# Kernel tuning notes

Hardware: AMD Instinct MI355X
Metric: run time of the kernel (lower is better)

Reference implementation:

```python
import jax, jax.numpy as jnp
import numpy as np

CODEBOOK_SIZE = 1024
LATENT_DIM = 256
COMMITMENT_COST = 0.25
EMA_DECAY = 0.99
EPS = 1e-05


def setup_inputs() -> dict:
    key = jax.random.key(0)
    k1, k2, k3 = jax.random.split(key, 3)
    B, D, T, K = 32, LATENT_DIM, 2048, CODEBOOK_SIZE
    z = jax.random.normal(k1, (B, D, T), dtype=jnp.float32)
    embedding = jax.random.normal(k2, (K, D), dtype=jnp.float32) * (1.0 / K)
    ema_count = jnp.ones((K,), dtype=jnp.float32)
    ema_weight = jax.random.normal(k3, (K, D), dtype=jnp.float32) * (1.0 / K)
    return {"z": z, "embedding": embedding, "ema_count": ema_count, "ema_weight": ema_weight}


def reference(z, embedding, ema_count, ema_weight):
    B, D, T = z.shape
    K = embedding.shape[0]
    # (B, D, T) -> (B*T, D)
    z_flat = jnp.transpose(z, (0, 2, 1)).reshape(-1, D)

    # Squared L2 distances: ||z||^2 + ||e||^2 - 2 z.e
    d = (jnp.sum(z_flat * z_flat, axis=1, keepdims=True)
         + jnp.sum(embedding * embedding, axis=1)[None, :]
         - 2.0 * (z_flat @ embedding.T))  # (N, K)
    token_ids_flat = jnp.argmin(d, axis=1)  # (N,)
    z_q_flat = embedding[token_ids_flat]    # (N, D)

    # Losses (stop_gradient mirrors .detach())
    commitment_loss = jnp.mean((z_flat - jax.lax.stop_gradient(z_q_flat)) ** 2)
    codebook_loss = jnp.mean((z_q_flat - jax.lax.stop_gradient(z_flat)) ** 2)
    vq_loss = codebook_loss + COMMITMENT_COST * commitment_loss

    # Straight-through estimator
    z_q_flat_ste = z_flat + jax.lax.stop_gradient(z_q_flat - z_flat)
    z_q = jnp.transpose(z_q_flat_ste.reshape(B, T, D), (0, 2, 1))
    token_ids = token_ids_flat.reshape(B, T)

    # EMA codebook update (training-mode, no-grad)
    zf = jax.lax.stop_gradient(z_flat)
    ids = jax.lax.stop_gradient(token_ids_flat)
    counts = jax.ops.segment_sum(jnp.ones_like(zf[:, 0]), ids, num_segments=K)  # (K,)
    sums = jax.ops.segment_sum(zf, ids, num_segments=K)                          # (K, D)
    new_ema_count = EMA_DECAY * ema_count + (1.0 - EMA_DECAY) * counts
    new_ema_weight = EMA_DECAY * ema_weight + (1.0 - EMA_DECAY) * sums
    n = jnp.sum(new_ema_count)
    smoothed = (new_ema_count + EPS) / (n + K * EPS) * n
    new_embedding = new_ema_weight / smoothed[:, None]

    return z_q, token_ids, vq_loss, new_embedding, new_ema_count, new_ema_weight
```

## Files before the change

kernel.cpp:

```cpp
#include <hip/hip_runtime.h>
#include <hip/hip_bf16.h>
#include <string.h>

#define D_ 256
#define K_ 1024
#define T_ 2048
#define B_ 32
#define N_ 65536

#define OFF_ZQ   0u
#define OFF_IDS  16777216u
#define OFF_LOSS 16842752u
#define OFF_EMB  16842753u
#define OFF_CNT  17104897u
#define OFF_W    17105921u

#define WS_IDS     0x000000u
#define WS_ZN      0x040000u
#define WS_ORDER   0x080000u
#define WS_SUMS    0x0C0000u
#define WS_COUNTS  0x1C0000u
#define WS_EN      0x1C1000u
#define WS_SM      0x1C2000u
#define WS_OFFS    0x1C3000u
#define WS_CURSOR  0x1C4000u
#define WS_LOSS    0x1C5000u
#define WS_END_SM  0x1C6000u
#define WS_ESPLIT  0x290000u
#define WS_TOP2    0x390000u
#define WS_ZSPLIT  0x1000000u
#define WS_END_XL  0x3000000u

#define TAU 2.0e-4f

typedef float f32x4 __attribute__((ext_vector_type(4)));
typedef _Float16 f16x8 __attribute__((ext_vector_type(8)));
typedef unsigned short ushort_t;
typedef unsigned long long u64;

static __device__ inline float fmul_rn_opaque(float a, float b) {
  float r = a * b;
  asm volatile("" : "+v"(r));
  return r;
}

static __device__ inline ushort_t f2h(float x) {
  _Float16 h = (_Float16)x;
  ushort_t u;
  __builtin_memcpy(&u, &h, 2);
  return u;
}
static __device__ inline float h2f(ushort_t u) {
  _Float16 h;
  __builtin_memcpy(&h, &u, 2);
  return (float)h;
}

static __device__ inline u64 skey(float s, int j) {
  unsigned int u = __float_as_uint(s);
  u = u ^ ((unsigned int)((int)u >> 31) | 0x80000000u);
  return ((u64)u << 32) | (unsigned int)j;
}
static __device__ inline float key_s(u64 k) {
  unsigned int u = (unsigned int)(k >> 32);
  u = (u & 0x80000000u) ? (u ^ 0x80000000u) : ~u;
  return __uint_as_float(u);
}

static __device__ __forceinline__ void gload16(const void* g, void* l) {
  __builtin_amdgcn_global_load_lds(
      (const __attribute__((address_space(1))) void*)g,
      (__attribute__((address_space(3))) void*)l, 16, 0, 0);
}

template <typename F>
static __device__ inline float np_pairwise256(F term) {
  float h0 = 0.f, h1 = 0.f;
#pragma unroll
  for (int half = 0; half < 2; ++half) {
    const int base = half * 128;
    float r[8];
#pragma unroll
    for (int k = 0; k < 8; ++k) r[k] = term(base + k);
    for (int i = 8; i < 128; i += 8) {
#pragma unroll
      for (int k = 0; k < 8; ++k) r[k] += term(base + i + k);
    }
    float v = ((r[0] + r[1]) + (r[2] + r[3])) + ((r[4] + r[5]) + (r[6] + r[7]));
    if (half == 0) h0 = v; else h1 = v;
  }
  return h0 + h1;
}

__global__ __launch_bounds__(256) void k_eprep(const float* __restrict__ emb,
                                               float* __restrict__ en,
                                               ushort_t* __restrict__ esplit) {
  const int tid = threadIdx.x;
  const int j = blockIdx.x * 32 + (tid >> 3);
  const int k = tid & 7;
  const float* e = emb + (size_t)j * D_;

  float h[2];
#pragma unroll
  for (int half = 0; half < 2; ++half) {
    float r = 0.f;
    for (int i = 0; i < 16; ++i) {
      float x = e[half * 128 + 8 * i + k];
      float t = fmul_rn_opaque(x, x);
      r = (i == 0) ? t : r + t;
    }
    float s = r + __shfl_xor(r, 1, 64);
    s = s + __shfl_xor(s, 2, 64);
    s = s + __shfl_xor(s, 4, 64);
    h[half] = s;
  }
  if (k == 0) en[j] = h[0] + h[1];

  ushort_t* er = esplit + (size_t)j * 256;
#pragma unroll
  for (int m = 0; m < 32; m += 4) {
    float4 v = *reinterpret_cast<const float4*>(e + k * 32 + m);
    *reinterpret_cast<ushort4*>(er + k * 32 + m) =
        make_ushort4(f2h(v.x * 256.f), f2h(v.y * 256.f),
                     f2h(v.z * 256.f), f2h(v.w * 256.f));
  }
}

__global__ __launch_bounds__(256) void k_zprep(const float* __restrict__ z,
                                               float* __restrict__ zn,
                                               ushort_t* __restrict__ zsplit) {
  __shared__ float tile[64][68];
  const int tid = threadIdx.x, bid = blockIdx.x;
  const int tchunk = bid & 31, b = bid >> 5;
  const int n0 = b * T_ + tchunk * 64;
  const int t4 = tid & 15, rq = tid >> 4;
  const int tok = tid >> 2, p = tid & 3;

  float r0 = 0.f, r1 = 0.f, h0 = 0.f;
  for (int c = 0; c < 4; ++c) {
    __syncthreads();
    const float* zp = z + (size_t)b * D_ * T_ + (size_t)(c * 64) * T_ + tchunk * 64;
#pragma unroll
    for (int i = 0; i < 4; ++i) {
      int dd = rq + 16 * i;
      *reinterpret_cast<float4*>(&tile[dd][t4 * 4]) =
          *reinterpret_cast<const float4*>(&zp[(size_t)dd * T_ + t4 * 4]);
    }
    __syncthreads();
    {
      ushort_t* dst = zsplit + (size_t)(n0 + tok) * 256 + c * 64 + p * 16;
      unsigned int wbuf[8];
#pragma unroll
      for (int jj = 0; jj < 16; jj += 2) {
        float x0 = tile[p * 16 + jj][tok];
        float x1 = tile[p * 16 + jj + 1][tok];
        wbuf[jj >> 1] = (unsigned int)f2h(x0) | ((unsigned int)f2h(x1) << 16);
      }
      *reinterpret_cast<uint4*>(dst) = make_uint4(wbuf[0], wbuf[1], wbuf[2], wbuf[3]);
      *reinterpret_cast<uint4*>(dst + 8) = make_uint4(wbuf[4], wbuf[5], wbuf[6], wbuf[7]);
    }
#pragma unroll
    for (int il = 0; il < 8; ++il) {
      float x0 = tile[8 * il + 2 * p][tok];
      float x1 = tile[8 * il + 2 * p + 1][tok];
      float t0 = fmul_rn_opaque(x0, x0);
      float t1 = fmul_rn_opaque(x1, x1);
      if ((c & 1) == 0 && il == 0) { r0 = t0; r1 = t1; }
      else { r0 += t0; r1 += t1; }
    }
    if (c & 1) {
      float s = r0 + r1;
      s = s + __shfl_xor(s, 1, 64);
      s = s + __shfl_xor(s, 2, 64);
      if (c == 1) h0 = s;
      else if (p == 0) zn[n0 + tok] = h0 + s;
    }
  }
}

static __device__ inline void top2merge(u64& k1, u64& k2, u64 o1, u64 o2) {
  if (o1 < k1) { u64 t = k1 < o2 ? k1 : o2; k2 = t; k1 = o1; }
  else { k2 = k2 < o1 ? k2 : o1; }
}

__global__ __launch_bounds__(512) void k_gemm(
    const ushort_t* __restrict__ zsplit, const ushort_t* __restrict__ esplit,
    const float* __restrict__ en, ulonglong2* __restrict__ top2) {
  __shared__ char ldsbuf[65536];

  const int tid = threadIdx.x;
  const int w = blockIdx.x;
  const int xcd = w & 7;
  const int local = w >> 3;
  const int tt = (xcd << 5) + (local >> 2);
  const int ct = local & 3;
  const int r0 = tt * 256, c0 = ct * 256;

  const int lane = tid & 63;
  const int wv = tid >> 6;
  const int wm = wv >> 2, wn = wv & 3;
  const int m16 = lane & 15;
  const int g = lane >> 4;
  const int gb = g << 4;

  const int rl = lane >> 3;
  const int vlane = rl * 512 + ((((lane & 7) << 4)) ^ (rl << 4));
  const char* gza = (const char*)zsplit + (size_t)(r0 + wv * 32) * 512 + vlane;
  const char* gea = (const char*)esplit + (size_t)(c0 + wv * 32) * 512 + vlane;

  f32x4 acc[8][4];
#pragma unroll
  for (int mi = 0; mi < 8; ++mi)
#pragma unroll
    for (int ni = 0; ni < 4; ++ni) acc[mi][ni] = f32x4{0.f, 0.f, 0.f, 0.f};

  auto STAGE = [&](int it_) {
    const int kb = it_ << 7;
    char* lz = ldsbuf + wv * 4096;
    char* le = ldsbuf + 32768 + wv * 4096;
    const char* ga = gza + kb;
    const char* ge = gea + kb;
#pragma unroll
    for (int i = 0; i < 4; ++i) {
      gload16(ga + i * 4096, lz + i * 1024);
      gload16(ge + i * 4096, le + i * 1024);
    }
  };

  STAGE(0);
  __builtin_amdgcn_sched_barrier(0);

  const char* Zb = ldsbuf;
  const char* Eb = ldsbuf + 32768;
  for (int it = 0; it < 4; ++it) {
    asm volatile("s_waitcnt vmcnt(0)" ::: "memory");
    __builtin_amdgcn_sched_barrier(0);
    __builtin_amdgcn_s_barrier();
    __builtin_amdgcn_sched_barrier(0);

#pragma unroll
    for (int ks = 0; ks < 2; ++ks) {
      f16x8 ef[8], zf[4];
#pragma unroll
      for (int mi = 0; mi < 8; ++mi) {
        int row = wm * 128 + mi * 16 + m16;
        ef[mi] = *reinterpret_cast<const f16x8*>(
            Eb + row * 128 + (((ks << 6) + gb) ^ ((row & 7) << 4)));
      }
#pragma unroll
      for (int ni = 0; ni < 4; ++ni) {
        int row = wn * 64 + ni * 16 + m16;
        zf[ni] = *reinterpret_cast<const f16x8*>(
            Zb + row * 128 + (((ks << 6) + gb) ^ ((row & 7) << 4)));
      }
#pragma unroll
      for (int mi = 0; mi < 8; ++mi)
#pragma unroll
        for (int ni = 0; ni < 4; ++ni)
          acc[mi][ni] = __builtin_amdgcn_mfma_f32_16x16x32_f16(
              ef[mi], zf[ni], acc[mi][ni], 0, 0, 0);
    }
    asm volatile("s_waitcnt lgkmcnt(0)" ::: "memory");
    __builtin_amdgcn_sched_barrier(0);
    __builtin_amdgcn_s_barrier();
    __builtin_amdgcn_sched_barrier(0);
    if (it < 3) STAGE(it + 1);
    __builtin_amdgcn_sched_barrier(0);
  }

  u64* pairbuf = (u64*)ldsbuf;
  float env[8][4];
#pragma unroll
  for (int mi = 0; mi < 8; ++mi)
#pragma unroll
    for (int rg = 0; rg < 4; ++rg)
      env[mi][rg] = en[c0 + wm * 128 + mi * 16 + g * 4 + rg];

#pragma unroll
  for (int ni = 0; ni < 4; ++ni) {
    const int tok = wn * 64 + ni * 16 + m16;
    u64 k1 = ~0ull, k2 = ~0ull;
#pragma unroll
    for (int mi = 0; mi < 8; ++mi) {
#pragma unroll
      for (int rg = 0; rg < 4; ++rg) {
        int j = c0 + wm * 128 + mi * 16 + g * 4 + rg;
        float s = env[mi][rg] - acc[mi][ni][rg] * 0.0078125f;
        u64 key = skey(s, j);
        if (key < k1) { k2 = k1; k1 = key; }
        else if (key < k2) { k2 = key; }
      }
    }
    u64 o1 = (u64)__shfl_xor((long long)k1, 16, 64);
    u64 o2 = (u64)__shfl_xor((long long)k2, 16, 64);
    top2merge(k1, k2, o1, o2);
    o1 = (u64)__shfl_xor((long long)k1, 32, 64);
    o2 = (u64)__shfl_xor((long long)k2, 32, 64);
    top2merge(k1, k2, o1, o2);
    if (g == 0) {
      pairbuf[(tok * 2 + wm) * 2 + 0] = k1;
      pairbuf[(tok * 2 + wm) * 2 + 1] = k2;
    }
  }
  __syncthreads();
  if (tid < 256) {
    u64 a1 = pairbuf[(tid * 2 + 0) * 2 + 0], a2 = pairbuf[(tid * 2 + 0) * 2 + 1];
    top2merge(a1, a2, pairbuf[(tid * 2 + 1) * 2 + 0], pairbuf[(tid * 2 + 1) * 2 + 1]);
    top2[(size_t)(r0 + tid) * 4 + ct] = make_ulonglong2(a1, a2);
  }
}

__global__ __launch_bounds__(256) void k_merge(
    const ulonglong2* __restrict__ top2, const float* __restrict__ z,
    const float* __restrict__ emb, const float* __restrict__ en,
    const float* __restrict__ zn, int* __restrict__ ids,
    float* __restrict__ counts, double* __restrict__ loss,
    float* __restrict__ out) {
  int n = blockIdx.x * 256 + threadIdx.x;
  const ulonglong2* tp = top2 + (size_t)n * 4;
  const float znv = zn[n];
  u64 k[8];
#pragma unroll
  for (int i = 0; i < 4; ++i) {
    ulonglong2 v = tp[i];
    k[2 * i] = v.x; k[2 * i + 1] = v.y;
  }
  u64 mn = k[0];
#pragma unroll
  for (int i = 1; i < 8; ++i) mn = k[i] < mn ? k[i] : mn;
  float lim = key_s(mn) + TAU;
  int cnt = 0;
  int cj[4] = {0, 0, 0, 0};
#pragma unroll
  for (int i = 0; i < 8; ++i) {
    if (key_s(k[i]) <= lim) {
      if (cnt < 4) cj[cnt] = (int)(k[i] & 1023u);
      cnt++;
    }
  }
  int jf;
  float loss_n;
  if (cnt == 1) {
    jf = (int)(mn & 1023u);
    loss_n = znv + key_s(mn);
  } else {
    int b = n >> 11, t = n & 2047;
    const float* zb = z + (size_t)b * (D_ * (size_t)T_) + t;
    const float* e0 = emb + (size_t)cj[0] * D_;
    const float* e1 = emb + (size_t)cj[1] * D_;
    const float* e2 = emb + (size_t)cj[2] * D_;
    const float* e3 = emb + (size_t)cj[3] * D_;
    float a0 = 0.f, a1 = 0.f, a2 = 0.f, a3 = 0.f;
    for (int d = 0; d < D_; ++d) {
      float zv = zb[(size_t)d * T_];
      a0 = fmaf(zv, e0[d], a0);
      a1 = fmaf(zv, e1[d], a1);
      a2 = fmaf(zv, e2[d], a2);
      a3 = fmaf(zv, e3[d], a3);
    }
    float av[4] = {a0, a1, a2, a3};
    u64 best = ~0ull;
#pragma unroll
    for (int c = 0; c < 4; ++c) {
      if (c < cnt) {
        float A = znv + en[cj[c]];
        float s = A - 2.0f * av[c];
        u64 key = skey(s, cj[c]);
        best = key < best ? key : best;
      }
    }
    jf = (int)(best & 1023u);
    loss_n = key_s(best);
  }
  ids[n] = jf;
  out[OFF_IDS + (unsigned)n] = (float)jf;
  unsafeAtomicAdd(&counts[jf], 1.0f);

  float acc = loss_n;
#pragma unroll
  for (int o = 32; o; o >>= 1) acc += __shfl_down(acc, o);
  __shared__ float ls[4];
  int tid = threadIdx.x;
  if ((tid & 63) == 0) ls[tid >> 6] = acc;
  __syncthreads();
  if (tid == 0)
    unsafeAtomicAdd(loss, (double)(ls[0] + ls[1] + ls[2] + ls[3]));
}

__global__ __launch_bounds__(1024) void k_offsets(const float* __restrict__ counts,
                                                  int* __restrict__ offs,
                                                  int* __restrict__ cursor) {
  int k = threadIdx.x;
  int c = (int)counts[k];
  __shared__ int s[1024];
  s[k] = c;
  __syncthreads();
  for (int off = 1; off < 1024; off <<= 1) {
    int v = (k >= off) ? s[k - off] : 0;
    __syncthreads();
    s[k] += v;
    __syncthreads();
  }
  int excl = s[k] - c;
  offs[k] = excl;
  cursor[k] = excl;
}

__global__ __launch_bounds__(256) void k_bucket(const int* __restrict__ ids,
                                                int* __restrict__ cursor,
                                                int* __restrict__ order) {
  int n = blockIdx.x * 256 + threadIdx.x;
  int id = ids[n] & 1023;
  int slot = atomicAdd(&cursor[id], 1);
  order[slot & (N_ - 1)] = (id << 16) | n;
}

__global__ __launch_bounds__(256) void k_sums_bf(const ushort_t* __restrict__ zsplit,
                                                 const int* __restrict__ order,
                                                 float* __restrict__ sums) {
  __shared__ int pk[128];
  const int tid = threadIdx.x;
  if (tid < 128) pk[tid] = order[blockIdx.x * 128 + tid];
  __syncthreads();
  const int half = tid >> 7;
  const int l = tid & 127;
  const int s0 = half * 64;
  float a0 = 0.f, a1 = 0.f;
  int cur = pk[s0] >> 16;
#pragma unroll 4
  for (int i = 0; i < 64; ++i) {
    int v = pk[s0 + i];
    int code = v >> 16;
    if (code != cur) {
      unsafeAtomicAdd(&sums[(size_t)cur * D_ + 2 * l], a0);
      unsafeAtomicAdd(&sums[(size_t)cur * D_ + 2 * l + 1], a1);
      a0 = 0.f; a1 = 0.f; cur = code;
    }
    const char* row = (const char*)zsplit + (size_t)(v & 0xFFFF) * 512;
    unsigned int hw = *reinterpret_cast<const unsigned int*>(row + 4 * l);
    a0 += h2f((ushort_t)(hw & 0xFFFF));
    a1 += h2f((ushort_t)(hw >> 16));
  }
  unsafeAtomicAdd(&sums[(size_t)cur * D_ + 2 * l], a0);
  unsafeAtomicAdd(&sums[(size_t)cur * D_ + 2 * l + 1], a1);
}

__global__ __launch_bounds__(256) void k_zq(
    const float* __restrict__ emb, const int* __restrict__ ids,
    float* __restrict__ out) {
  __shared__ float tile[64][68];
  const int tid = threadIdx.x;
  const int bid = blockIdx.x;
  const int tchunk = bid & 31;
  const int dchunk = (bid >> 5) & 3;
  const int b = bid >> 7;
  const int n0 = b * T_ + tchunk * 64;
  {
    int tok = tid >> 2, part = tid & 3;
    int id = ids[n0 + tok] & 1023;
    const float* er = emb + (size_t)id * D_ + dchunk * 64 + part * 16;
#pragma unroll
    for (int k = 0; k < 4; ++k) {
      float4 v = *reinterpret_cast<const float4*>(er + 4 * k);
      int d = part * 16 + 4 * k;
      tile[d + 0][tok] = v.x; tile[d + 1][tok] = v.y;
      tile[d + 2][tok] = v.z; tile[d + 3][tok] = v.w;
    }
  }
  __syncthreads();
  const int t4 = tid & 15, dq = tid >> 4;
  const size_t zbase = (size_t)b * D_ * T_ + (size_t)(dchunk * 64) * T_ + tchunk * 64;
#pragma unroll
  for (int i = 0; i < 4; ++i) {
    int dd = dq + 16 * i;
    size_t a = zbase + (size_t)dd * T_ + t4 * 4;
    *reinterpret_cast<float4*>(out + OFF_ZQ + a) =
        *reinterpret_cast<const float4*>(&tile[dd][t4 * 4]);
  }
}

__global__ __launch_bounds__(256) void k_weight(
    const float* __restrict__ ema_count, const float* __restrict__ counts,
    const float* __restrict__ ema_weight, const float* __restrict__ sums,
    const double* __restrict__ loss, float* __restrict__ out) {
  const int k = blockIdx.x;
  const int tid = threadIdx.x;
  __shared__ float red[4];

  float part = 0.f;
#pragma unroll
  for (int i = 0; i < 4; ++i) {
    int idx = tid + 256 * i;
    part += 0.99f * ema_count[idx] + 0.01f * counts[idx];
  }
#pragma unroll
  for (int o = 32; o; o >>= 1) part += __shfl_down(part, o);
  if ((tid & 63) == 0) red[tid >> 6] = part;
  __syncthreads();
  float n = red[0] + red[1] + red[2] + red[3];

  float nck = 0.99f * ema_count[k] + 0.01f * counts[k];
  float smo = (nck + 1.0e-5f) / (n + 1024.0f * 1.0e-5f) * n;

  int i = k * 256 + tid;
  float w = 0.99f * ema_weight[i] + 0.01f * sums[i];
  out[OFF_W + i] = w;
  out[OFF_EMB + i] = w / smo;
  if (tid == 0) {
    out[OFF_CNT + k] = nck;
    if (k == 0) {
      double mean = loss[0] / 16777216.0;
      out[OFF_LOSS] = (float)(1.25 * mean);
    }
  }
}

__global__ __launch_bounds__(256) void k_en(const float* __restrict__ emb,
                                            float* __restrict__ en) {
  int j = blockIdx.x * 256 + threadIdx.x;
  const float* e = emb + (size_t)j * D_;
  en[j] = np_pairwise256([&](int d) { float x = e[d]; return fmul_rn_opaque(x, x); });
}

__global__ __launch_bounds__(256) void k_zn(const float* __restrict__ z,
                                            float* __restrict__ zn) {
  int n = blockIdx.x * 256 + threadIdx.x;
  int b = n >> 11, t = n & 2047;
  const float* zp = z + (size_t)b * (D_ * (size_t)T_) + t;
  zn[n] = np_pairwise256([&](int d) {
    float x = zp[(size_t)d * T_];
    return fmul_rn_opaque(x, x);
  });
}

__global__ __launch_bounds__(256) void k_assign(
    const float* __restrict__ z, const float* __restrict__ emb,
    const float* __restrict__ en, const float* __restrict__ zn,
    int* __restrict__ ids, float* __restrict__ counts,
    float* __restrict__ out) {
  __shared__ float zs[16][128];
  __shared__ float es[16][128];
  const int tid = threadIdx.x;
  const int tx = tid & 31;
  const int ty = tid >> 5;
  const int r0 = blockIdx.x * 128;
  const int b  = r0 >> 11;
  const int t0 = r0 & 2047;
  const float* zb = z + (size_t)b * (D_ * (size_t)T_) + t0;
  u64 keys[16];
#pragma unroll
  for (int r = 0; r < 16; ++r) keys[r] = ~0ull;
  for (int jc = 0; jc < K_; jc += 128) {
    float acc[16][4];
#pragma unroll
    for (int r = 0; r < 16; ++r)
#pragma unroll
      for (int c = 0; c < 4; ++c) acc[r][c] = 0.f;
    for (int d0 = 0; d0 < D_; d0 += 16) {
      __syncthreads();
#pragma unroll
      for (int i = 0; i < 2; ++i) {
        int slot = tid + 256 * i;
        int dd = slot >> 5, t4 = slot & 31;
        *reinterpret_cast<float4*>(&zs[dd][t4 * 4]) =
            *reinterpret_cast<const float4*>(&zb[(size_t)(d0 + dd) * T_ + t4 * 4]);
      }
#pragma unroll
      for (int i = 0; i < 2; ++i) {
        int slot = tid + 256 * i;
        int c = slot & 127, g = slot >> 7;
        int dd0 = g * 4;
        float4 ev = *reinterpret_cast<const float4*>(
            &emb[(size_t)(jc + c) * D_ + d0 + dd0]);
        es[dd0 + 0][c] = ev.x; es[dd0 + 1][c] = ev.y;
        es[dd0 + 2][c] = ev.z; es[dd0 + 3][c] = ev.w;
      }
      __syncthreads();
#pragma unroll
      for (int dd = 0; dd < 16; ++dd) {
        float4 e4 = *reinterpret_cast<const float4*>(&es[dd][tx * 4]);
        float4 z0 = *reinterpret_cast<const float4*>(&zs[dd][ty * 16]);
        float4 z1 = *reinterpret_cast<const float4*>(&zs[dd][ty * 16 + 4]);
        float4 z2 = *reinterpret_cast<const float4*>(&zs[dd][ty * 16 + 8]);
        float4 z3 = *reinterpret_cast<const float4*>(&zs[dd][ty * 16 + 12]);
        float zr[16] = {z0.x, z0.y, z0.z, z0.w, z1.x, z1.y, z1.z, z1.w,
                        z2.x, z2.y, z2.z, z2.w, z3.x, z3.y, z3.z, z3.w};
        float ec[4] = {e4.x, e4.y, e4.z, e4.w};
#pragma unroll
        for (int r = 0; r < 16; ++r)
#pragma unroll
          for (int c = 0; c < 4; ++c) acc[r][c] += zr[r] * ec[c];
      }
    }
#pragma unroll
    for (int r = 0; r < 16; ++r) {
      float znp = zn[r0 + ty * 16 + r];
      u64 kk = keys[r];
#pragma unroll
      for (int c = 0; c < 4; ++c) {
        int j = jc + tx * 4 + c;
        float A = znp + en[j];
        float s = A - 2.0f * acc[r][c];
        u64 key = skey(s, j);
        kk = key < kk ? key : kk;
      }
      keys[r] = kk;
    }
  }
#pragma unroll
  for (int r = 0; r < 16; ++r) {
    u64 kk = keys[r];
#pragma unroll
    for (int m = 1; m < 32; m <<= 1) {
      u64 o = (u64)__shfl_xor((long long)kk, m, 32);
      kk = o < kk ? o : kk;
    }
    keys[r] = kk;
  }
  if ((tid & 31) == 0) {
#pragma unroll
    for (int r = 0; r < 16; ++r) {
      int n = r0 + ty * 16 + r;
      int jf = (int)(keys[r] & 1023u);
      ids[n] = jf;
      out[OFF_IDS + (unsigned)n] = (float)jf;
      unsafeAtomicAdd(&counts[jf], 1.0f);
    }
  }
}

__global__ __launch_bounds__(256) void k_scatter_atomic(
    const float* __restrict__ z, const float* __restrict__ emb,
    const int* __restrict__ ids, float* __restrict__ sums,
    double* __restrict__ loss, float* __restrict__ out) {
  const int tid = threadIdx.x;
  unsigned int gi = blockIdx.x * 256u + (unsigned int)tid;
  int t4 = (int)(gi & 511u);
  int bd = (int)(gi >> 9);
  int d  = bd & 255;
  int b  = bd >> 8;
  size_t base = (size_t)bd * T_ + (size_t)t4 * 4;
  const float4 zv = *reinterpret_cast<const float4*>(z + base);
  const int tb = b * T_ + t4 * 4;
  float zz[4] = {zv.x, zv.y, zv.z, zv.w};
  float e4[4];
  float acc = 0.f;
#pragma unroll
  for (int u = 0; u < 4; ++u) {
    int id = ids[tb + u] & 1023;
    float e = emb[(size_t)id * D_ + d];
    float df = zz[u] - e;
    acc += df * df;
    e4[u] = e;
    unsafeAtomicAdd(&sums[(size_t)id * D_ + d], zz[u]);
  }
  *reinterpret_cast<float4*>(out + OFF_ZQ + base) =
      make_float4(e4[0], e4[1], e4[2], e4[3]);
#pragma unroll
  for (int o = 32; o; o >>= 1) acc += __shfl_down(acc, o);
  __shared__ float ls[4];
  int lane = tid & 63, wid = tid >> 6;
  if (lane == 0) ls[wid] = acc;
  __syncthreads();
  if (tid == 0) unsafeAtomicAdd(loss, (double)(ls[0] + ls[1] + ls[2] + ls[3]));
}

__global__ __launch_bounds__(1024) void k_count_fb(
    const float* __restrict__ ema_count, const float* __restrict__ counts,
    float* __restrict__ sm, const double* __restrict__ loss,
    float* __restrict__ out) {
  int k = threadIdx.x;
  float nc = 0.99f * ema_count[k] + 0.01f * counts[k];
  __shared__ float red[1024];
  red[k] = nc;
  __syncthreads();
  for (int s = 512; s > 0; s >>= 1) {
    if (k < s) red[k] += red[k + s];
    __syncthreads();
  }
  float n = red[0];
  float smo = (nc + 1.0e-5f) / (n + 1024.0f * 1.0e-5f) * n;
  sm[k] = smo;
  out[OFF_CNT + k] = nc;
  if (k == 0) {
    double mean = loss[0] / 16777216.0;
    out[OFF_LOSS] = (float)(1.25 * mean);
  }
}

__global__ __launch_bounds__(256) void k_weight_fb(
    const float* __restrict__ ema_weight, const float* __restrict__ sums,
    const float* __restrict__ sm, float* __restrict__ out) {
  int i = blockIdx.x * 256 + threadIdx.x;
  int k = i >> 8;
  float w = 0.99f * ema_weight[i] + 0.01f * sums[i];
  out[OFF_W + i] = w;
  out[OFF_EMB + i] = w / sm[k];
}

extern "C" void kernel_launch(void* const* d_in, const int* in_sizes, int n_in,
                              void* d_out, int out_size, void* d_ws, size_t ws_size,
                              hipStream_t stream) {
  const float* z          = (const float*)d_in[0];
  const float* emb        = (const float*)d_in[1];
  const float* ema_count  = (const float*)d_in[2];
  const float* ema_weight = (const float*)d_in[3];
  float* out = (float*)d_out;
  char* ws = (char*)d_ws;
  if (ws_size < (size_t)WS_END_SM) return;

  int*    ids    = (int*)(ws + WS_IDS);
  float*  zn     = (float*)(ws + WS_ZN);
  int*    order  = (int*)(ws + WS_ORDER);
  float*  sums   = (float*)(ws + WS_SUMS);
  float*  counts = (float*)(ws + WS_COUNTS);
  float*  en     = (float*)(ws + WS_EN);
  float*  sm     = (float*)(ws + WS_SM);
  int*    offs   = (int*)(ws + WS_OFFS);
  int*    cursor = (int*)(ws + WS_CURSOR);
  double* loss   = (double*)(ws + WS_LOSS);

  hipMemsetAsync(ws + WS_SUMS, 0, WS_END_SM - WS_SUMS, stream);

  if (ws_size >= (size_t)WS_END_XL) {
    ushort_t*   esplit = (ushort_t*)(ws + WS_ESPLIT);
    ushort_t*   zsplit = (ushort_t*)(ws + WS_ZSPLIT);
    ulonglong2* top2   = (ulonglong2*)(ws + WS_TOP2);

    k_eprep  <<<K_ / 32, 256, 0, stream>>>(emb, en, esplit);
    k_zprep  <<<B_ * (T_ / 64), 256, 0, stream>>>(z, zn, zsplit);
    k_gemm   <<<(K_ / 256) * (N_ / 256), 512, 0, stream>>>(zsplit, esplit, en, top2);
    k_merge  <<<N_ / 256, 256, 0, stream>>>(top2, z, emb, en, zn, ids, counts, loss, out);
    k_offsets<<<1, 1024, 0, stream>>>(counts, offs, cursor);
    k_bucket <<<N_ / 256, 256, 0, stream>>>(ids, cursor, order);
    k_sums_bf<<<N_ / 128, 256, 0, stream>>>(zsplit, order, sums);
    k_zq     <<<B_ * (D_ / 64) * (T_ / 64), 256, 0, stream>>>(emb, ids, out);
    k_weight <<<K_, 256, 0, stream>>>(ema_count, counts, ema_weight, sums, loss, out);
  } else {
    k_en <<<K_ / 256, 256, 0, stream>>>(emb, en);
    k_zn <<<N_ / 256, 256, 0, stream>>>(z, zn);
    k_assign<<<N_ / 128, 256, 0, stream>>>(z, emb, en, zn, ids, counts, out);
    k_scatter_atomic<<<(N_ * (D_ / 4)) / 256, 256, 0, stream>>>(z, emb, ids, sums, loss, out);
    k_count_fb <<<1, 1024, 0, stream>>>(ema_count, counts, sm, loss, out);
    k_weight_fb<<<(K_ * D_) / 256, 256, 0, stream>>>(ema_weight, sums, sm, out);
  }
}
```

Baseline: 181.7 us.

## Fuse top-2 merge and z_q gather into GEMM kernel, loop over codebook tiles

Each GEMM block now covers all 1024 codebook entries for its 256 tokens by looping over four column tiles, instead of one tile per block. Per-tile top-2 candidates stay in LDS, so the final argmin, refinement, loss and count updates run inside the same kernel, along with the transposed z_q write. This removes the top2 workspace round trip and two kernel launches. In exchange the grid shrinks from 1024 to 256 blocks, leaving fewer blocks to fill the GPU and less parallelism. The z_q write stage and the global tail now run serially at the end of each block.

```diff
diff --git a/kernel.cpp b/kernel.cpp
--- a/kernel.cpp
+++ b/kernel.cpp
@@ -27,7 +27,6 @@
 #define WS_LOSS    0x1C5000u
 #define WS_END_SM  0x1C6000u
 #define WS_ESPLIT  0x290000u
-#define WS_TOP2    0x390000u
 #define WS_ZSPLIT  0x1000000u
 #define WS_END_XL  0x3000000u
 
@@ -185,16 +184,20 @@
 
 __global__ __launch_bounds__(512) void k_gemm(
     const ushort_t* __restrict__ zsplit, const ushort_t* __restrict__ esplit,
-    const float* __restrict__ en, ulonglong2* __restrict__ top2) {
+    const float* __restrict__ en, const float* __restrict__ zn,
+    const float* __restrict__ z, const float* __restrict__ emb,
+    int* __restrict__ ids, float* __restrict__ counts,
+    double* __restrict__ loss, float* __restrict__ out) {
   __shared__ char ldsbuf[65536];
+  __shared__ u64 ldsK[256][16];
+  __shared__ int idsl[256];
+  __shared__ float ls[8];
 
   const int tid = threadIdx.x;
   const int w = blockIdx.x;
   const int xcd = w & 7;
-  const int local = w >> 3;
-  const int tt = (xcd << 5) + (local >> 2);
-  const int ct = local & 3;
-  const int r0 = tt * 256, c0 = ct * 256;
+  const int tt = (xcd << 5) + (w >> 3);
+  const int r0 = tt * 256;
 
   const int lane = tid & 63;
   const int wv = tid >> 6;
@@ -206,185 +209,212 @@
   const int rl = lane >> 3;
   const int vlane = rl * 512 + ((((lane & 7) << 4)) ^ (rl << 4));
   const char* gza = (const char*)zsplit + (size_t)(r0 + wv * 32) * 512 + vlane;
-  const char* gea = (const char*)esplit + (size_t)(c0 + wv * 32) * 512 + vlane;
-
-  f32x4 acc[8][4];
-#pragma unroll
-  for (int mi = 0; mi < 8; ++mi)
-#pragma unroll
-    for (int ni = 0; ni < 4; ++ni) acc[mi][ni] = f32x4{0.f, 0.f, 0.f, 0.f};
-
-  auto STAGE = [&](int it_) {
-    const int kb = it_ << 7;
-    char* lz = ldsbuf + wv * 4096;
-    char* le = ldsbuf + 32768 + wv * 4096;
-    const char* ga = gza + kb;
-    const char* ge = gea + kb;
-#pragma unroll
-    for (int i = 0; i < 4; ++i) {
-      gload16(ga + i * 4096, lz + i * 1024);
-      gload16(ge + i * 4096, le + i * 1024);
-    }
-  };
-
-  STAGE(0);
-  __builtin_amdgcn_sched_barrier(0);
+  const char* geabase = (const char*)esplit + (size_t)(wv * 32) * 512 + vlane;
 
   const char* Zb = ldsbuf;
   const char* Eb = ldsbuf + 32768;
-  for (int it = 0; it < 4; ++it) {
-    asm volatile("s_waitcnt vmcnt(0)" ::: "memory");
+
+  for (int ct = 0; ct < 4; ++ct) {
+    const int c0 = ct * 256;
+    const char* gea = geabase + (size_t)c0 * 512;
+
+    f32x4 acc[8][4];
+#pragma unroll
+    for (int mi = 0; mi < 8; ++mi)
+#pragma unroll
+      for (int ni = 0; ni < 4; ++ni) acc[mi][ni] = f32x4{0.f, 0.f, 0.f, 0.f};
+
+    auto STAGE = [&](int it_) {
+      const int kb = it_ << 7;
+      char* lz = ldsbuf + wv * 4096;
+      char* le = ldsbuf + 32768 + wv * 4096;
+#pragma unroll
+      for (int i = 0; i < 4; ++i) {
+        gload16(gza + kb + i * 4096, lz + i * 1024);
+        gload16(gea + kb + i * 4096, le + i * 1024);
+      }
+    };
+
+    STAGE(0);
     __builtin_amdgcn_sched_barrier(0);
-    __builtin_amdgcn_s_barrier();
-    __builtin_amdgcn_sched_barrier(0);
-
-#pragma unroll
-    for (int ks = 0; ks < 2; ++ks) {
-      f16x8 ef[8], zf[4];
+
+    for (int it = 0; it < 4; ++it) {
+      asm volatile("s_waitcnt vmcnt(0)" ::: "memory");
+      __builtin_amdgcn_sched_barrier(0);
+      __builtin_amdgcn_s_barrier();
+      __builtin_amdgcn_sched_barrier(0);
+
+#pragma unroll
+      for (int ks = 0; ks < 2; ++ks) {
+        f16x8 ef[8], zf[4];
+#pragma unroll
+        for (int mi = 0; mi < 8; ++mi) {
+          int row = wm * 128 + mi * 16 + m16;
+          ef[mi] = *reinterpret_cast<const f16x8*>(
+              Eb + row * 128 + (((ks << 6) + gb) ^ ((row & 7) << 4)));
+        }
+#pragma unroll
+        for (int ni = 0; ni < 4; ++ni) {
+          int row = wn * 64 + ni * 16 + m16;
+          zf[ni] = *reinterpret_cast<const f16x8*>(
+              Zb + row * 128 + (((ks << 6) + gb) ^ ((row & 7) << 4)));
+        }
+#pragma unroll
+        for (int mi = 0; mi < 8; ++mi)
+#pragma unroll
+          for (int ni = 0; ni < 4; ++ni)
+            acc[mi][ni] = __builtin_amdgcn_mfma_f32_16x16x32_f16(
+                ef[mi], zf[ni], acc[mi][ni], 0, 0, 0);
+      }
+      asm volatile("s_waitcnt lgkmcnt(0)" ::: "memory");
+      __builtin_amdgcn_sched_barrier(0);
+      __builtin_amdgcn_s_barrier();
+      __builtin_amdgcn_sched_barrier(0);
+      if (it < 3) STAGE(it + 1);
+      __builtin_amdgcn_sched_barrier(0);
+    }
+
+    float env[8][4];
+#pragma unroll
+    for (int mi = 0; mi < 8; ++mi)
+#pragma unroll
+      for (int rg = 0; rg < 4; ++rg)
+        env[mi][rg] = en[c0 + wm * 128 + mi * 16 + g * 4 + rg];
+
+#pragma unroll
+    for (int ni = 0; ni < 4; ++ni) {
+      const int tok = wn * 64 + ni * 16 + m16;
+      u64 k1 = ~0ull, k2 = ~0ull;
 #pragma unroll
       for (int mi = 0; mi < 8; ++mi) {
-        int row = wm * 128 + mi * 16 + m16;
-        ef[mi] = *reinterpret_cast<const f16x8*>(
-            Eb + row * 128 + (((ks << 6) + gb) ^ ((row & 7) << 4)));
-      }
-#pragma unroll
-      for (int ni = 0; ni < 4; ++ni) {
-        int row = wn * 64 + ni * 16 + m16;
-        zf[ni] = *reinterpret_cast<const f16x8*>(
-            Zb + row * 128 + (((ks << 6) + gb) ^ ((row & 7) << 4)));
-      }
-#pragma unroll
-      for (int mi = 0; mi < 8; ++mi)
-#pragma unroll
-        for (int ni = 0; ni < 4; ++ni)
-          acc[mi][ni] = __builtin_amdgcn_mfma_f32_16x16x32_f16(
-              ef[mi], zf[ni], acc[mi][ni], 0, 0, 0);
-    }
-    asm volatile("s_waitcnt lgkmcnt(0)" ::: "memory");
-    __builtin_amdgcn_sched_barrier(0);
-    __builtin_amdgcn_s_barrier();
-    __builtin_amdgcn_sched_barrier(0);
-    if (it < 3) STAGE(it + 1);
-    __builtin_amdgcn_sched_barrier(0);
-  }
-
-  u64* pairbuf = (u64*)ldsbuf;
-  float env[8][4];
-#pragma unroll
-  for (int mi = 0; mi < 8; ++mi)
-#pragma unroll
-    for (int rg = 0; rg < 4; ++rg)
-      env[mi][rg] = en[c0 + wm * 128 + mi * 16 + g * 4 + rg];
-
-#pragma unroll
-  for (int ni = 0; ni < 4; ++ni) {
-    const int tok = wn * 64 + ni * 16 + m16;
-    u64 k1 = ~0ull, k2 = ~0ull;
-#pragma unroll
-    for (int mi = 0; mi < 8; ++mi) {
-#pragma unroll
-      for (int rg = 0; rg < 4; ++rg) {
-        int j = c0 + wm * 128 + mi * 16 + g * 4 + rg;
-        float s = env[mi][rg] - acc[mi][ni][rg] * 0.0078125f;
-        u64 key = skey(s, j);
-        if (key < k1) { k2 = k1; k1 = key; }
-        else if (key < k2) { k2 = key; }
-      }
-    }
-    u64 o1 = (u64)__shfl_xor((long long)k1, 16, 64);
-    u64 o2 = (u64)__shfl_xor((long long)k2, 16, 64);
-    top2merge(k1, k2, o1, o2);
-    o1 = (u64)__shfl_xor((long long)k1, 32, 64);
-    o2 = (u64)__shfl_xor((long long)k2, 32, 64);
-    top2merge(k1, k2, o1, o2);
-    if (g == 0) {
-      pairbuf[(tok * 2 + wm) * 2 + 0] = k1;
-      pairbuf[(tok * 2 + wm) * 2 + 1] = k2;
+#pragma unroll
+        for (int rg = 0; rg < 4; ++rg) {
+          int j = c0 + wm * 128 + mi * 16 + g * 4 + rg;
+          float s = env[mi][rg] - acc[mi][ni][rg] * 0.0078125f;
+          u64 key = skey(s, j);
+          if (key < k1) { k2 = k1; k1 = key; }
+          else if (key < k2) { k2 = key; }
+        }
+      }
+      u64 o1 = (u64)__shfl_xor((long long)k1, 16, 64);
+      u64 o2 = (u64)__shfl_xor((long long)k2, 16, 64);
+      top2merge(k1, k2, o1, o2);
+      o1 = (u64)__shfl_xor((long long)k1, 32, 64);
+      o2 = (u64)__shfl_xor((long long)k2, 32, 64);
+      top2merge(k1, k2, o1, o2);
+      if (g == 0) {
+        ldsK[tok][ct * 4 + wm * 2 + 0] = k1;
+        ldsK[tok][ct * 4 + wm * 2 + 1] = k2;
+      }
     }
   }
   __syncthreads();
+
+  float loss_n = 0.f;
   if (tid < 256) {
-    u64 a1 = pairbuf[(tid * 2 + 0) * 2 + 0], a2 = pairbuf[(tid * 2 + 0) * 2 + 1];
-    top2merge(a1, a2, pairbuf[(tid * 2 + 1) * 2 + 0], pairbuf[(tid * 2 + 1) * 2 + 1]);
-    top2[(size_t)(r0 + tid) * 4 + ct] = make_ulonglong2(a1, a2);
-  }
-}
-
-__global__ __launch_bounds__(256) void k_merge(
-    const ulonglong2* __restrict__ top2, const float* __restrict__ z,
-    const float* __restrict__ emb, const float* __restrict__ en,
-    const float* __restrict__ zn, int* __restrict__ ids,
-    float* __restrict__ counts, double* __restrict__ loss,
-    float* __restrict__ out) {
-  int n = blockIdx.x * 256 + threadIdx.x;
-  const ulonglong2* tp = top2 + (size_t)n * 4;
-  const float znv = zn[n];
-  u64 k[8];
-#pragma unroll
-  for (int i = 0; i < 4; ++i) {
-    ulonglong2 v = tp[i];
-    k[2 * i] = v.x; k[2 * i + 1] = v.y;
-  }
-  u64 mn = k[0];
-#pragma unroll
-  for (int i = 1; i < 8; ++i) mn = k[i] < mn ? k[i] : mn;
-  float lim = key_s(mn) + TAU;
-  int cnt = 0;
-  int cj[4] = {0, 0, 0, 0};
-#pragma unroll
-  for (int i = 0; i < 8; ++i) {
-    if (key_s(k[i]) <= lim) {
-      if (cnt < 4) cj[cnt] = (int)(k[i] & 1023u);
-      cnt++;
-    }
-  }
-  int jf;
-  float loss_n;
-  if (cnt == 1) {
-    jf = (int)(mn & 1023u);
-    loss_n = znv + key_s(mn);
-  } else {
-    int b = n >> 11, t = n & 2047;
-    const float* zb = z + (size_t)b * (D_ * (size_t)T_) + t;
-    const float* e0 = emb + (size_t)cj[0] * D_;
-    const float* e1 = emb + (size_t)cj[1] * D_;
-    const float* e2 = emb + (size_t)cj[2] * D_;
-    const float* e3 = emb + (size_t)cj[3] * D_;
-    float a0 = 0.f, a1 = 0.f, a2 = 0.f, a3 = 0.f;
-    for (int d = 0; d < D_; ++d) {
-      float zv = zb[(size_t)d * T_];
-      a0 = fmaf(zv, e0[d], a0);
-      a1 = fmaf(zv, e1[d], a1);
-      a2 = fmaf(zv, e2[d], a2);
-      a3 = fmaf(zv, e3[d], a3);
-    }
-    float av[4] = {a0, a1, a2, a3};
-    u64 best = ~0ull;
-#pragma unroll
-    for (int c = 0; c < 4; ++c) {
-      if (c < cnt) {
-        float A = znv + en[cj[c]];
-        float s = A - 2.0f * av[c];
-        u64 key = skey(s, cj[c]);
-        best = key < best ? key : best;
-      }
-    }
-    jf = (int)(best & 1023u);
-    loss_n = key_s(best);
-  }
-  ids[n] = jf;
-  out[OFF_IDS + (unsigned)n] = (float)jf;
-  unsafeAtomicAdd(&counts[jf], 1.0f);
-
-  float acc = loss_n;
-#pragma unroll
-  for (int o = 32; o; o >>= 1) acc += __shfl_down(acc, o);
-  __shared__ float ls[4];
-  int tid = threadIdx.x;
-  if ((tid & 63) == 0) ls[tid >> 6] = acc;
+    const int n = r0 + tid;
+    const float znv = zn[n];
+    u64 k[16];
+#pragma unroll
+    for (int i = 0; i < 16; ++i) k[i] = ldsK[tid][i];
+    u64 mn = k[0];
+#pragma unroll
+    for (int i = 1; i < 16; ++i) mn = k[i] < mn ? k[i] : mn;
+    float lim = key_s(mn) + TAU;
+    int cnt = 0;
+    int cj[4] = {0, 0, 0, 0};
+#pragma unroll
+    for (int i = 0; i < 16; ++i) {
+      if (key_s(k[i]) <= lim) {
+        if (cnt < 4) cj[cnt] = (int)(k[i] & 1023u);
+        cnt++;
+      }
+    }
+    int jf;
+    if (cnt == 1) {
+      jf = (int)(mn & 1023u);
+      loss_n = znv + key_s(mn);
+    } else {
+      int b = n >> 11, t = n & 2047;
+      const float* zb = z + (size_t)b * (D_ * (size_t)T_) + t;
+      const float* e0 = emb + (size_t)cj[0] * D_;
+      const float* e1 = emb + (size_t)cj[1] * D_;
+      const float* e2 = emb + (size_t)cj[2] * D_;
+      const float* e3 = emb + (size_t)cj[3] * D_;
+      float a0 = 0.f, a1 = 0.f, a2 = 0.f, a3 = 0.f;
+      for (int d = 0; d < D_; ++d) {
+        float zv = zb[(size_t)d * T_];
+        a0 = fmaf(zv, e0[d], a0);
+        a1 = fmaf(zv, e1[d], a1);
+        a2 = fmaf(zv, e2[d], a2);
+        a3 = fmaf(zv, e3[d], a3);
+      }
+      float av[4] = {a0, a1, a2, a3};
+      u64 best = ~0ull;
+#pragma unroll
+      for (int c = 0; c < 4; ++c) {
+        if (c < cnt) {
+          float A = znv + en[cj[c]];
+          float s = A - 2.0f * av[c];
+          u64 key = skey(s, cj[c]);
+          best = key < best ? key : best;
+        }
+      }
+      jf = (int)(best & 1023u);
+      loss_n = key_s(best);
+    }
+    ids[n] = jf;
+    out[OFF_IDS + (unsigned)n] = (float)jf;
+    idsl[tid] = jf;
+    unsafeAtomicAdd(&counts[jf], 1.0f);
+  }
+  {
+    float accl = loss_n;
+#pragma unroll
+    for (int o = 32; o; o >>= 1) accl += __shfl_down(accl, o);
+    if ((tid & 63) == 0) ls[tid >> 6] = accl;
+  }
   __syncthreads();
-  if (tid == 0)
-    unsafeAtomicAdd(loss, (double)(ls[0] + ls[1] + ls[2] + ls[3]));
+  if (tid == 0) {
+    float t = ls[0] + ls[1] + ls[2] + ls[3] + ls[4] + ls[5] + ls[6] + ls[7];
+    unsafeAtomicAdd(loss, (double)t);
+  }
+
+  const int half = tid >> 8;
+  const int ltid = tid & 255;
+  float (*tile)[68] = reinterpret_cast<float(*)[68]>(ldsbuf + half * 17408);
+  const int zb_ = r0 >> 11;
+  const int t0_ = r0 & 2047;
+  for (int st = 0; st < 8; ++st) {
+    int s = st * 2 + half;
+    int tg = s >> 2, dchunk = s & 3;
+    {
+      int tok = ltid >> 2, part = ltid & 3;
+      int id = idsl[tg * 64 + tok] & 1023;
+      const float* er = emb + (size_t)id * D_ + dchunk * 64 + part * 16;
+#pragma unroll
+      for (int kk = 0; kk < 4; ++kk) {
+        float4 v = *reinterpret_cast<const float4*>(er + 4 * kk);
+        int d = part * 16 + 4 * kk;
+        tile[d + 0][tok] = v.x; tile[d + 1][tok] = v.y;
+        tile[d + 2][tok] = v.z; tile[d + 3][tok] = v.w;
+      }
+    }
+    __syncthreads();
+    {
+      const int t4 = ltid & 15, dq = ltid >> 4;
+      const size_t zbase = (size_t)zb_ * D_ * T_ + (size_t)(dchunk * 64) * T_ +
+                           (size_t)(t0_ + tg * 64);
+#pragma unroll
+      for (int i = 0; i < 4; ++i) {
+        int dd = dq + 16 * i;
+        size_t a = zbase + (size_t)dd * T_ + t4 * 4;
+        *reinterpret_cast<float4*>(out + OFF_ZQ + a) =
+            *reinterpret_cast<const float4*>(&tile[dd][t4 * 4]);
+      }
+    }
+    __syncthreads();
+  }
 }
 
 __global__ __launch_bounds__(1024) void k_offsets(const float* __restrict__ counts,
@@ -445,40 +475,6 @@
   unsafeAtomicAdd(&sums[(size_t)cur * D_ + 2 * l + 1], a1);
 }
 
-__global__ __launch_bounds__(256) void k_zq(
-    const float* __restrict__ emb, const int* __restrict__ ids,
-    float* __restrict__ out) {
-  __shared__ float tile[64][68];
-  const int tid = threadIdx.x;
-  const int bid = blockIdx.x;
-  const int tchunk = bid & 31;
-  const int dchunk = (bid >> 5) & 3;
-  const int b = bid >> 7;
-  const int n0 = b * T_ + tchunk * 64;
-  {
-    int tok = tid >> 2, part = tid & 3;
-    int id = ids[n0 + tok] & 1023;
-    const float* er = emb + (size_t)id * D_ + dchunk * 64 + part * 16;
-#pragma unroll
-    for (int k = 0; k < 4; ++k) {
-      float4 v = *reinterpret_cast<const float4*>(er + 4 * k);
-      int d = part * 16 + 4 * k;
-      tile[d + 0][tok] = v.x; tile[d + 1][tok] = v.y;
-      tile[d + 2][tok] = v.z; tile[d + 3][tok] = v.w;
-    }
-  }
-  __syncthreads();
-  const int t4 = tid & 15, dq = tid >> 4;
-  const size_t zbase = (size_t)b * D_ * T_ + (size_t)(dchunk * 64) * T_ + tchunk * 64;
-#pragma unroll
-  for (int i = 0; i < 4; ++i) {
-    int dd = dq + 16 * i;
-    size_t a = zbase + (size_t)dd * T_ + t4 * 4;
-    *reinterpret_cast<float4*>(out + OFF_ZQ + a) =
-        *reinterpret_cast<const float4*>(&tile[dd][t4 * 4]);
-  }
-}
-
 __global__ __launch_bounds__(256) void k_weight(
     const float* __restrict__ ema_count, const float* __restrict__ counts,
     const float* __restrict__ ema_weight, const float* __restrict__ sums,
@@ -723,18 +719,16 @@
   hipMemsetAsync(ws + WS_SUMS, 0, WS_END_SM - WS_SUMS, stream);
 
   if (ws_size >= (size_t)WS_END_XL) {
-    ushort_t*   esplit = (ushort_t*)(ws + WS_ESPLIT);
-    ushort_t*   zsplit = (ushort_t*)(ws + WS_ZSPLIT);
-    ulonglong2* top2   = (ulonglong2*)(ws + WS_TOP2);
+    ushort_t* esplit = (ushort_t*)(ws + WS_ESPLIT);
+    ushort_t* zsplit = (ushort_t*)(ws + WS_ZSPLIT);
 
     k_eprep  <<<K_ / 32, 256, 0, stream>>>(emb, en, esplit);
     k_zprep  <<<B_ * (T_ / 64), 256, 0, stream>>>(z, zn, zsplit);
-    k_gemm   <<<(K_ / 256) * (N_ / 256), 512, 0, stream>>>(zsplit, esplit, en, top2);
-    k_merge  <<<N_ / 256, 256, 0, stream>>>(top2, z, emb, en, zn, ids, counts, loss, out);
+    k_gemm   <<<N_ / 256, 512, 0, stream>>>(zsplit, esplit, en, zn, z, emb,
+                                            ids, counts, loss, out);
     k_offsets<<<1, 1024, 0, stream>>>(counts, offs, cursor);
     k_bucket <<<N_ / 256, 256, 0, stream>>>(ids, cursor, order);
     k_sums_bf<<<N_ / 128, 256, 0, stream>>>(zsplit, order, sums);
-    k_zq     <<<B_ * (D_ / 64) * (T_ / 64), 256, 0, stream>>>(emb, ids, out);
     k_weight <<<K_, 256, 0, stream>>>(ema_count, counts, ema_weight, sums, loss, out);
   } else {
     k_en <<<K_ / 256, 256, 0, stream>>>(emb, en);
```

Result: slower. 187.2 us (+3.1%).
